# Performance work log

Measured on AMD Instinct MI355X. Metric: run time of the kernel, lower is better.

The kernel has to match this reference:

```python
import jax, jax.numpy as jnp
import numpy as np

TEMPERATURE = 0.2
EPS = 1e-10

def setup_inputs() -> dict:
    key = jax.random.key(0)
    x = jax.random.normal(key, (8, 1024, 64, 64), dtype=jnp.float32)
    return {"x": x}

def reference(x):
    B, C, H, W = x.shape
    xf = x.reshape(B, C, H * W)                      # [B, C, HW]
    dot = jnp.einsum('bcn,bdn->bcd', xf, xf) / TEMPERATURE  # [B, C, C]
    logits = jax.nn.softmax(dot, axis=-1)
    diag = jnp.diagonal(logits, axis1=-2, axis2=-1)  # [B, C]
    loss = -jnp.log(diag + EPS)
    return jnp.mean(loss)
```

## Files before the change

### kernel.cpp

```cpp
#include <hip/hip_runtime.h>
#include <hip/hip_bf16.h>

#define BATCH 8
#define CCH 1024
#define NHW 4096
#define SCALE 5.0f
#define ROWS (BATCH * CCH)

typedef unsigned char u8;
typedef unsigned int u32;
typedef __attribute__((ext_vector_type(4))) float float4v;

__device__ __forceinline__ void async_load16(const void* gsrc, void* ldst) {
    __builtin_amdgcn_global_load_lds(
        (__attribute__((address_space(1))) void*)gsrc,
        (__attribute__((address_space(3))) void*)ldst,
        16, 0, 0);
}

__device__ __forceinline__ u32 pk4_fp8(float a, float b, float c, float d) {
    u32 v = __builtin_amdgcn_cvt_pk_fp8_f32(a, b, 0, false);
    v = __builtin_amdgcn_cvt_pk_fp8_f32(c, d, v, true);
    return v;
}

__device__ __forceinline__ float ssq4_fp8(u32 q) {
    float d0 = __builtin_amdgcn_cvt_f32_fp8(q, 0);
    float d1 = __builtin_amdgcn_cvt_f32_fp8(q, 1);
    float d2 = __builtin_amdgcn_cvt_f32_fp8(q, 2);
    float d3 = __builtin_amdgcn_cvt_f32_fp8(q, 3);
    return d0 * d0 + d1 * d1 + d2 * d2 + d3 * d3;
}

template <bool CONVERT>
__global__ __launch_bounds__(256) void prep_kernel(const float* __restrict__ x,
                                                   u8* __restrict__ xq,
                                                   float* __restrict__ diag,
                                                   float* __restrict__ l_acc) {
    const int row = blockIdx.x;
    const int tid = threadIdx.x;
    const float* src = x + (size_t)row * NHW;
    float ssum = 0.f;
#pragma unroll
    for (int p = 0; p < 4; ++p) {
        const int idx = p * 1024 + tid * 4;
        float4 v = *(const float4*)(src + idx);
        const u32 q = pk4_fp8(v.x, v.y, v.z, v.w);
        ssum += ssq4_fp8(q);
        if (CONVERT) *(u32*)(xq + (size_t)row * NHW + idx) = q;
    }
#pragma unroll
    for (int m = 1; m < 64; m <<= 1) ssum += __shfl_xor(ssum, m);
    __shared__ float red[4];
    if ((tid & 63) == 0) red[tid >> 6] = ssum;
    __syncthreads();
    if (tid == 0) {
        diag[row] = (red[0] + red[1] + red[2] + red[3]) * SCALE;
        l_acc[row] = 0.f;
    }
}

template <bool QSRC>
__global__ __launch_bounds__(256) void gram_kernel(const u8* __restrict__ Xq,
                                                   const float* __restrict__ Xf,
                                                   const float* __restrict__ diag,
                                                   float* __restrict__ l_acc,
                                                   float* __restrict__ num) {
    __shared__ __align__(16) u8 As[16384];
    __shared__ __align__(16) u8 Bs[8192];

    const int bid = blockIdx.x;
    const int b = bid & 7;
    const int t = bid >> 3;

    int bi = 0;
#pragma unroll
    for (int i = 7; i >= 1; --i) {
        if (t >= i * (17 - i)) { bi = i; break; }
    }
    const int bj2 = 2 * bi + (t - bi * (17 - bi));
    const bool aliasB = (bj2 == 2 * bi) || (bj2 == 2 * bi + 1);

    const int tid  = threadIdx.x;
    const int lane = tid & 63;
    const int w    = tid >> 6;
    const int wm   = w >> 1;
    const int wn   = w & 1;

    const int st_r  = lane >> 3;
    const int st_kc = (lane & 7) ^ st_r;

    const u8*    pA  = nullptr; const u8*    pB  = nullptr;
    const float* pAf = nullptr; const float* pBf = nullptr;
    if (QSRC) {
        const u8* baseX = Xq + (size_t)b * CCH * NHW;
        pA = baseX + (size_t)(bi * 128 + w * 32 + st_r) * NHW + st_kc * 16;
        pB = baseX + (size_t)(bj2 * 64 + w * 16 + st_r) * NHW + st_kc * 16;
    } else {
        const float* baseXf = Xf + (size_t)b * CCH * NHW;
        pAf = baseXf + (size_t)(bi * 128 + w * 32 + st_r) * NHW + st_kc * 16;
        pBf = baseXf + (size_t)(bj2 * 64 + w * 16 + st_r) * NHW + st_kc * 16;
    }

    float4v acc[4][2] = {};

    for (int K0 = 0; K0 < NHW; K0 += 128) {
        __syncthreads();
        if (QSRC) {
#pragma unroll
            for (int t8 = 0; t8 < 4; ++t8)
                async_load16(pA + (size_t)(t8 * 8) * NHW + K0,
                             As + (size_t)(w * 32 + t8 * 8) * 128);
            if (!aliasB) {
#pragma unroll
                for (int t8 = 0; t8 < 2; ++t8)
                    async_load16(pB + (size_t)(t8 * 8) * NHW + K0,
                                 Bs + (size_t)(w * 16 + t8 * 8) * 128);
            }
        } else {
#pragma unroll
            for (int t8 = 0; t8 < 4; ++t8) {
                const float* s = pAf + (size_t)(t8 * 8) * NHW + K0;
                float4 f0 = *(const float4*)(s);
                float4 f1 = *(const float4*)(s + 4);
                float4 f2 = *(const float4*)(s + 8);
                float4 f3 = *(const float4*)(s + 12);
                u32* d = (u32*)(As + (size_t)(w * 32 + t8 * 8 + st_r) * 128 + (lane & 7) * 16);
                d[0] = pk4_fp8(f0.x, f0.y, f0.z, f0.w);
                d[1] = pk4_fp8(f1.x, f1.y, f1.z, f1.w);
                d[2] = pk4_fp8(f2.x, f2.y, f2.z, f2.w);
                d[3] = pk4_fp8(f3.x, f3.y, f3.z, f3.w);
            }
            if (!aliasB) {
#pragma unroll
                for (int t8 = 0; t8 < 2; ++t8) {
                    const float* s = pBf + (size_t)(t8 * 8) * NHW + K0;
                    float4 f0 = *(const float4*)(s);
                    float4 f1 = *(const float4*)(s + 4);
                    float4 f2 = *(const float4*)(s + 8);
                    float4 f3 = *(const float4*)(s + 12);
                    u32* d = (u32*)(Bs + (size_t)(w * 16 + t8 * 8 + st_r) * 128 + (lane & 7) * 16);
                    d[0] = pk4_fp8(f0.x, f0.y, f0.z, f0.w);
                    d[1] = pk4_fp8(f1.x, f1.y, f1.z, f1.w);
                    d[2] = pk4_fp8(f2.x, f2.y, f2.z, f2.w);
                    d[3] = pk4_fp8(f3.x, f3.y, f3.z, f3.w);
                }
            }
        }
        __syncthreads();

        const u8* Bbase = aliasB ? (As + (size_t)(bj2 - 2 * bi) * 64 * 128) : Bs;
        const int q  = lane >> 4;
        const int rl = lane & 15;
#pragma unroll
        for (int s = 0; s < 4; ++s) {
            const int cbase = 2 * s + (q >> 1);
            const int off8  = (q & 1) * 8;
            long af[4], bf[2];
#pragma unroll
            for (int mt = 0; mt < 4; ++mt)
                af[mt] = *(const long*)(As + (size_t)(wm * 64 + mt * 16 + rl) * 128
                                           + (size_t)(cbase ^ (rl & 7)) * 16 + off8);
#pragma unroll
            for (int nt = 0; nt < 2; ++nt)
                bf[nt] = *(const long*)(Bbase + (size_t)(wn * 32 + nt * 16 + rl) * 128
                                              + (size_t)(cbase ^ (rl & 7)) * 16 + off8);
#pragma unroll
            for (int mt = 0; mt < 4; ++mt)
#pragma unroll
                for (int nt = 0; nt < 2; ++nt)
                    acc[mt][nt] = __builtin_amdgcn_mfma_f32_16x16x32_fp8_fp8(af[mt], bf[nt], acc[mt][nt], 0, 0, 0);
        }
    }

    const int q  = lane >> 4;
    const int cl = lane & 15;
    const int rowbase = bi * 128 + wm * 64;
    const int colbase = bj2 * 64 + wn * 32;
    const float* dgb = diag + b * CCH;
    float* lb = l_acc + b * CCH;

#pragma unroll
    for (int mt = 0; mt < 4; ++mt) {
#pragma unroll
        for (int reg = 0; reg < 4; ++reg) {
            const int gr = rowbase + mt * 16 + q * 4 + reg;
            const float dg = dgb[gr];
            float s = 0.f;
#pragma unroll
            for (int nt = 0; nt < 2; ++nt) {
                const int gc = colbase + nt * 16 + cl;
                const float e = __expf(acc[mt][nt][reg] * SCALE - dg);
                if (gr <= gc) s += e;
                if (gr == gc) num[b * CCH + gr] = e;
            }
            s += __shfl_xor(s, 1);
            s += __shfl_xor(s, 2);
            s += __shfl_xor(s, 4);
            s += __shfl_xor(s, 8);
            if (cl == 0) atomicAdd(lb + gr, s);
        }
    }

#pragma unroll
    for (int nt = 0; nt < 2; ++nt) {
        const int gc = colbase + nt * 16 + cl;
        const float dgc = dgb[gc];
        float s = 0.f;
#pragma unroll
        for (int mt = 0; mt < 4; ++mt) {
#pragma unroll
            for (int reg = 0; reg < 4; ++reg) {
                const int gr = rowbase + mt * 16 + q * 4 + reg;
                if (gr < gc) s += __expf(acc[mt][nt][reg] * SCALE - dgc);
            }
        }
        s += __shfl_xor(s, 16);
        s += __shfl_xor(s, 32);
        if (lane < 16) atomicAdd(lb + gc, s);
    }
}

__global__ __launch_bounds__(1024) void finalize_kernel(const float* __restrict__ l_acc,
                                                        const float* __restrict__ num,
                                                        float* __restrict__ out) {
    const int tid = threadIdx.x;
    float s = 0.f;
    for (int r = tid; r < ROWS; r += 1024) {
        const float d = num[r] / l_acc[r];
        s += -__logf(d + 1e-10f);
    }
#pragma unroll
    for (int m = 1; m < 64; m <<= 1) s += __shfl_xor(s, m);
    __shared__ float red[16];
    if ((tid & 63) == 0) red[tid >> 6] = s;
    __syncthreads();
    if (tid == 0) {
        float tot = 0.f;
#pragma unroll
        for (int i = 0; i < 16; ++i) tot += red[i];
        out[0] = tot * (1.0f / (float)ROWS);
    }
}

extern "C" void kernel_launch(void* const* d_in, const int* in_sizes, int n_in,
                              void* d_out, int out_size, void* d_ws, size_t ws_size,
                              hipStream_t stream) {
    const float* x = (const float*)d_in[0];
    float* out = (float*)d_out;

    const size_t xq_bytes   = (size_t)BATCH * CCH * NHW;
    const size_t stat_bytes = (size_t)ROWS * 4;
    const bool fast = ws_size >= xq_bytes + 3 * stat_bytes;

    const int ntiles = 72;

    if (fast) {
        u8*    xq    = (u8*)d_ws;
        float* diag  = (float*)((char*)d_ws + xq_bytes);
        float* l_acc = diag + ROWS;
        float* num   = l_acc + ROWS;
        prep_kernel<true><<<ROWS, 256, 0, stream>>>(x, xq, diag, l_acc);
        gram_kernel<true><<<BATCH * ntiles, 256, 0, stream>>>(xq, nullptr, diag, l_acc, num);
        finalize_kernel<<<1, 1024, 0, stream>>>(l_acc, num, out);
    } else {
        float* diag  = (float*)d_ws;
        float* l_acc = diag + ROWS;
        float* num   = l_acc + ROWS;
        prep_kernel<false><<<ROWS, 256, 0, stream>>>(x, nullptr, diag, l_acc);
        gram_kernel<false><<<BATCH * ntiles, 256, 0, stream>>>(nullptr, x, diag, l_acc, num);
        finalize_kernel<<<1, 1024, 0, stream>>>(l_acc, num, out);
    }
}
```

Baseline: 243.1 us.

## Double-buffer LDS tiles in gram kernel to overlap loads with MFMA

```diff
diff --git a/kernel.cpp b/kernel.cpp
--- a/kernel.cpp
+++ b/kernel.cpp
@@ -10,6 +10,7 @@
 typedef unsigned char u8;
 typedef unsigned int u32;
 typedef __attribute__((ext_vector_type(4))) float float4v;
+typedef __attribute__((ext_vector_type(4))) u32 uint4v;
 
 __device__ __forceinline__ void async_load16(const void* gsrc, void* ldst) {
     __builtin_amdgcn_global_load_lds(
@@ -66,8 +67,8 @@
                                                    const float* __restrict__ diag,
                                                    float* __restrict__ l_acc,
                                                    float* __restrict__ num) {
-    __shared__ __align__(16) u8 As[16384];
-    __shared__ __align__(16) u8 Bs[8192];
+    __shared__ __align__(16) u8 As[2][16384];
+    __shared__ __align__(16) u8 Bs[2][8192];
 
     const int bid = blockIdx.x;
     const int b = bid & 7;
@@ -104,18 +105,17 @@
 
     float4v acc[4][2] = {};
 
-    for (int K0 = 0; K0 < NHW; K0 += 128) {
-        __syncthreads();
+    auto stage = [&](int buf, int K0) {
         if (QSRC) {
 #pragma unroll
             for (int t8 = 0; t8 < 4; ++t8)
                 async_load16(pA + (size_t)(t8 * 8) * NHW + K0,
-                             As + (size_t)(w * 32 + t8 * 8) * 128);
+                             As[buf] + (size_t)(w * 32 + t8 * 8) * 128);
             if (!aliasB) {
 #pragma unroll
                 for (int t8 = 0; t8 < 2; ++t8)
                     async_load16(pB + (size_t)(t8 * 8) * NHW + K0,
-                                 Bs + (size_t)(w * 16 + t8 * 8) * 128);
+                                 Bs[buf] + (size_t)(w * 16 + t8 * 8) * 128);
             }
         } else {
 #pragma unroll
@@ -125,11 +125,12 @@
                 float4 f1 = *(const float4*)(s + 4);
                 float4 f2 = *(const float4*)(s + 8);
                 float4 f3 = *(const float4*)(s + 12);
-                u32* d = (u32*)(As + (size_t)(w * 32 + t8 * 8 + st_r) * 128 + (lane & 7) * 16);
-                d[0] = pk4_fp8(f0.x, f0.y, f0.z, f0.w);
-                d[1] = pk4_fp8(f1.x, f1.y, f1.z, f1.w);
-                d[2] = pk4_fp8(f2.x, f2.y, f2.z, f2.w);
-                d[3] = pk4_fp8(f3.x, f3.y, f3.z, f3.w);
+                uint4v d;
+                d.x = pk4_fp8(f0.x, f0.y, f0.z, f0.w);
+                d.y = pk4_fp8(f1.x, f1.y, f1.z, f1.w);
+                d.z = pk4_fp8(f2.x, f2.y, f2.z, f2.w);
+                d.w = pk4_fp8(f3.x, f3.y, f3.z, f3.w);
+                *(uint4v*)(As[buf] + (size_t)(w * 32 + t8 * 8 + st_r) * 128 + (lane & 7) * 16) = d;
             }
             if (!aliasB) {
 #pragma unroll
@@ -139,38 +140,47 @@
                     float4 f1 = *(const float4*)(s + 4);
                     float4 f2 = *(const float4*)(s + 8);
                     float4 f3 = *(const float4*)(s + 12);
-                    u32* d = (u32*)(Bs + (size_t)(w * 16 + t8 * 8 + st_r) * 128 + (lane & 7) * 16);
-                    d[0] = pk4_fp8(f0.x, f0.y, f0.z, f0.w);
-                    d[1] = pk4_fp8(f1.x, f1.y, f1.z, f1.w);
-                    d[2] = pk4_fp8(f2.x, f2.y, f2.z, f2.w);
-                    d[3] = pk4_fp8(f3.x, f3.y, f3.z, f3.w);
+                    uint4v d;
+                    d.x = pk4_fp8(f0.x, f0.y, f0.z, f0.w);
+                    d.y = pk4_fp8(f1.x, f1.y, f1.z, f1.w);
+                    d.z = pk4_fp8(f2.x, f2.y, f2.z, f2.w);
+                    d.w = pk4_fp8(f3.x, f3.y, f3.z, f3.w);
+                    *(uint4v*)(Bs[buf] + (size_t)(w * 16 + t8 * 8 + st_r) * 128 + (lane & 7) * 16) = d;
                 }
             }
         }
-        __syncthreads();
-
-        const u8* Bbase = aliasB ? (As + (size_t)(bj2 - 2 * bi) * 64 * 128) : Bs;
+    };
+
+    stage(0, 0);
+    __syncthreads();
+
+    for (int i = 0; i < NHW / 128; ++i) {
+        const int cur = i & 1;
+        const int K0n = (i + 1) * 128;
+        if (K0n < NHW) stage(cur ^ 1, K0n);
+
+        const u8* Ab = As[cur];
+        const u8* Bb = aliasB ? (Ab + (size_t)(bj2 - 2 * bi) * 64 * 128) : Bs[cur];
         const int q  = lane >> 4;
         const int rl = lane & 15;
 #pragma unroll
         for (int s = 0; s < 4; ++s) {
             const int cbase = 2 * s + (q >> 1);
-            const int off8  = (q & 1) * 8;
+            const int boff  = (int)((cbase ^ (rl & 7)) * 16 + (q & 1) * 8);
             long af[4], bf[2];
 #pragma unroll
             for (int mt = 0; mt < 4; ++mt)
-                af[mt] = *(const long*)(As + (size_t)(wm * 64 + mt * 16 + rl) * 128
-                                           + (size_t)(cbase ^ (rl & 7)) * 16 + off8);
+                af[mt] = *(const long*)(Ab + (size_t)(wm * 64 + mt * 16 + rl) * 128 + boff);
 #pragma unroll
             for (int nt = 0; nt < 2; ++nt)
-                bf[nt] = *(const long*)(Bbase + (size_t)(wn * 32 + nt * 16 + rl) * 128
-                                              + (size_t)(cbase ^ (rl & 7)) * 16 + off8);
+                bf[nt] = *(const long*)(Bb + (size_t)(wn * 32 + nt * 16 + rl) * 128 + boff);
 #pragma unroll
             for (int mt = 0; mt < 4; ++mt)
 #pragma unroll
                 for (int nt = 0; nt < 2; ++nt)
                     acc[mt][nt] = __builtin_amdgcn_mfma_f32_16x16x32_fp8_fp8(af[mt], bf[nt], acc[mt][nt], 0, 0, 0);
         }
+        __syncthreads();
     }
 
     const int q  = lane >> 4;
```

After: 241.0 us. No clear change (-0.9%).
